# Kernel tuning notes

Hardware: AMD Instinct MI355X
Metric: run time of the kernel (lower is better)

The kernel has to match this reference:

```python
import jax, jax.numpy as jnp
import numpy as np
import math

DIM = 1024
HEADS = 16
DIM_HEAD = 64
INNER = HEADS * DIM_HEAD
NUM_BUCKETS = 32
MAX_DISTANCE = 128


def setup_inputs() -> dict:
    key = jax.random.key(0)
    ks = jax.random.split(key, 6)
    x = jax.random.normal(ks[0], (2, 2048, DIM), dtype=jnp.float32)
    Wq = jax.random.normal(ks[1], (DIM, INNER), dtype=jnp.float32) * (DIM ** -0.5)
    Wkv = jax.random.normal(ks[2], (DIM, 2 * DIM_HEAD), dtype=jnp.float32) * (DIM ** -0.5)
    Wout = jax.random.normal(ks[3], (INNER, DIM), dtype=jnp.float32) * (INNER ** -0.5)
    bout = jnp.zeros((DIM,), dtype=jnp.float32)
    rel_emb = jax.random.normal(ks[4], (NUM_BUCKETS, HEADS), dtype=jnp.float32) * 0.02
    return {"x": x, "Wq": Wq, "Wkv": Wkv, "Wout": Wout, "bout": bout, "rel_emb": rel_emb}


def _relative_position_bucket(rel_pos, num_buckets=NUM_BUCKETS, max_distance=MAX_DISTANCE):
    # rel_pos: [i, j] int32, k_pos - q_pos
    n = jnp.maximum(-rel_pos, 0)
    max_exact = num_buckets // 2
    is_small = n < max_exact
    n_safe = jnp.maximum(n, 1)  # avoid log(0); masked by is_small anyway
    val_if_large = max_exact + (
        jnp.log(n_safe.astype(jnp.float32) / max_exact)
        / math.log(max_distance / max_exact)
        * (num_buckets - max_exact)
    ).astype(jnp.int32)
    val_if_large = jnp.minimum(val_if_large, num_buckets - 1)
    return jnp.where(is_small, n, val_if_large)


def reference(x, Wq, Wkv, Wout, bout, rel_emb):
    b, n, _ = x.shape
    scale = DIM_HEAD ** -0.5
    bias_scale = DIM_HEAD ** 0.5

    q = (x @ Wq).reshape(b, n, HEADS, DIM_HEAD).transpose(0, 2, 1, 3) * scale  # [b,h,n,d]
    kv = x @ Wkv  # [b,n,2d]
    k, v = kv[..., :DIM_HEAD], kv[..., DIM_HEAD:]  # shared single-head K/V [b,n,d]

    sim = jnp.einsum('bhid,bjd->bhij', q, k)

    # T5 relative position bias
    pos = jnp.arange(n, dtype=jnp.int32)
    rel_pos = pos[None, :] - pos[:, None]  # [i,j] = k_pos - q_pos
    rp_bucket = _relative_position_bucket(rel_pos)
    bias = rel_emb[rp_bucket]  # [i,j,h]
    sim = sim + jnp.transpose(bias, (2, 0, 1))[None] * bias_scale

    # causal mask: mask strictly-upper triangle
    causal_mask = jnp.triu(jnp.ones((n, n), dtype=bool), k=1)
    neg = jnp.finfo(sim.dtype).max
    sim = jnp.where(causal_mask[None, None], -neg, sim)

    attn = jax.nn.softmax(sim, axis=-1)
    out = jnp.einsum('bhij,bjd->bhid', attn, v)
    out = out.transpose(0, 2, 1, 3).reshape(b, n, INNER)
    return out @ Wout + bout
```

## Files before the change

### kernel.cpp

```cpp
#include <hip/hip_runtime.h>
#include <cstdint>
#include <cmath>

typedef _Float16 half8 __attribute__((ext_vector_type(8)));
typedef unsigned short ushort8 __attribute__((ext_vector_type(8)));
typedef float floatx4 __attribute__((ext_vector_type(4)));

#define VT_STRIDE 2080

__device__ __forceinline__ unsigned short f2h(float f) {
    union { _Float16 h; unsigned short u; } cv;
    cv.h = (_Float16)f;
    return cv.u;
}

__device__ __forceinline__ void gld_lds16(const unsigned short* g, unsigned short* l) {
    __builtin_amdgcn_global_load_lds(
        (const __attribute__((address_space(1))) unsigned int*)g,
        (__attribute__((address_space(3))) unsigned int*)l, 16, 0, 0);
}

__global__ void prep_kernel(const float* __restrict__ x,
                            const float* __restrict__ Wq, const float* __restrict__ Wkv,
                            const float* __restrict__ Wout,
                            unsigned short* __restrict__ xh,
                            unsigned short* __restrict__ Wqkvt, unsigned short* __restrict__ Wot) {
    int bxi = blockIdx.x;
    if (bxi >= 68) {
        int fb = (bxi - 68) * 32 + blockIdx.y;
        int tt = threadIdx.y * 32 + threadIdx.x;
        int idx = fb * 256 + tt;
        const float4* p = (const float4*)x;
        float4 a = p[idx * 2], b = p[idx * 2 + 1];
        ushort8 o;
        o[0] = f2h(a.x); o[1] = f2h(a.y); o[2] = f2h(a.z); o[3] = f2h(a.w);
        o[4] = f2h(b.x); o[5] = f2h(b.y); o[6] = f2h(b.z); o[7] = f2h(b.w);
        *(ushort8*)(xh + (size_t)idx * 8) = o;
        return;
    }
    __shared__ float tile[32][33];
    const float* in; unsigned short* out; int C; int cb;
    if (bxi < 32)      { in = Wq;   out = Wqkvt;                 C = 1024; cb = bxi; }
    else if (bxi < 36) { in = Wkv;  out = Wqkvt + 1024 * 1024;   C = 128;  cb = bxi - 32; }
    else               { in = Wout; out = Wot;                   C = 1024; cb = bxi - 36; }
    int bx = cb * 32, by = blockIdx.y * 32;
    int xx = threadIdx.x, y0 = threadIdx.y;
    #pragma unroll
    for (int k = 0; k < 4; k++) {
        int y = y0 + k * 8;
        tile[y][xx] = in[(size_t)(by + y) * C + bx + xx];
    }
    __syncthreads();
    #pragma unroll
    for (int k = 0; k < 4; k++) {
        int y = y0 + k * 8;
        out[(size_t)(bx + y) * 1024 + by + xx] = f2h(tile[xx][y]);
    }
}

template<int MODE>
__global__ __launch_bounds__(256) void gemm_mn(
    const unsigned short* __restrict__ A, const unsigned short* __restrict__ Bt,
    unsigned short* __restrict__ oq, unsigned short* __restrict__ ok,
    unsigned short* __restrict__ ov, float* __restrict__ of,
    const float* __restrict__ bias)
{
    __shared__ __align__(16) unsigned short As[2][64 * 64];
    __shared__ __align__(16) unsigned short Bs[2][64 * 64];
    const int K = 1024;
    int t = threadIdx.x;
    int w = t >> 6, lane = t & 63, g = lane >> 4, il = lane & 15;
    int wr = w >> 1, wc = w & 1;
    int m0 = blockIdx.x * 64, n0 = blockIdx.y * 64;

    int l8 = lane >> 3, b8 = lane & 7;
    int swz = (b8 ^ l8) * 8;
    const unsigned short* Ag = A  + (size_t)(m0 + w * 16 + l8) * K + swz;
    const unsigned short* Bg = Bt + (size_t)(n0 + w * 16 + l8) * K + swz;
    int e0 = (g ^ (il & 7)) * 8;

    floatx4 acc[2][2] = {};

    #pragma unroll
    for (int q = 0; q < 2; q++) {
        gld_lds16(Ag + (size_t)(q * 8) * K, &As[0][(w * 16 + q * 8) * 64]);
        gld_lds16(Bg + (size_t)(q * 8) * K, &Bs[0][(w * 16 + q * 8) * 64]);
    }

    int cb = 0;
    for (int k0 = 0; k0 < K; k0 += 64, cb ^= 1) {
        if (k0 + 64 < K) {
            #pragma unroll
            for (int q = 0; q < 2; q++) {
                gld_lds16(Ag + (size_t)(q * 8) * K + k0 + 64, &As[cb ^ 1][(w * 16 + q * 8) * 64]);
                gld_lds16(Bg + (size_t)(q * 8) * K + k0 + 64, &Bs[cb ^ 1][(w * 16 + q * 8) * 64]);
            }
            asm volatile("s_waitcnt vmcnt(4)" ::: "memory");
        } else {
            asm volatile("s_waitcnt vmcnt(0)" ::: "memory");
        }
        __builtin_amdgcn_s_barrier();
        __builtin_amdgcn_sched_barrier(0);

        const unsigned short* Ac = &As[cb][0];
        const unsigned short* Bc = &Bs[cb][0];
        #pragma unroll
        for (int ks = 0; ks < 2; ks++) {
            half8 a[2];
            #pragma unroll
            for (int mt = 0; mt < 2; mt++)
                a[mt] = *(const half8*)&Ac[(wr * 32 + mt * 16 + il) * 64 + (e0 ^ (ks * 32))];
            #pragma unroll
            for (int nt = 0; nt < 2; nt++) {
                half8 b = *(const half8*)&Bc[(wc * 32 + nt * 16 + il) * 64 + (e0 ^ (ks * 32))];
                #pragma unroll
                for (int mt = 0; mt < 2; mt++)
                    acc[mt][nt] = __builtin_amdgcn_mfma_f32_16x16x32_f16(a[mt], b, acc[mt][nt], 0, 0, 0);
            }
        }
        asm volatile("s_waitcnt lgkmcnt(0)" ::: "memory");
        __builtin_amdgcn_s_barrier();
    }

    #pragma unroll
    for (int mt = 0; mt < 2; mt++) {
        #pragma unroll
        for (int nt = 0; nt < 2; nt++) {
            #pragma unroll
            for (int r = 0; r < 4; r++) {
                int row = m0 + wr * 32 + mt * 16 + 4 * g + r;
                int col = n0 + wc * 32 + nt * 16 + il;
                float v = acc[mt][nt][r];
                if (MODE == 0) {
                    if (col < 1024) {
                        int b = row >> 11, i = row & 2047, h = col >> 6, d = col & 63;
                        oq[(size_t)((b * 16 + h) * 2048 + i) * 64 + d] = f2h(v * 0.18033688011112042f);
                    } else if (col < 1088) {
                        ok[(size_t)row * 64 + (col - 1024)] = f2h(v);
                    } else {
                        int b = row >> 11, j = row & 2047;
                        ov[(size_t)((b << 6) + (col - 1088)) * VT_STRIDE + j] = f2h(v);
                    }
                } else {
                    of[(size_t)row * 1024 + col] = v + bias[col];
                }
            }
        }
    }
}

__global__ __launch_bounds__(256) void attn_kernel(
    const unsigned short* __restrict__ qh, const unsigned short* __restrict__ kh,
    const unsigned short* __restrict__ vt, const float* __restrict__ rel_emb,
    unsigned short* __restrict__ ob)
{
    __shared__ float bias_tab[256];
    __shared__ __align__(16) unsigned short Ks[2][64 * 64];
    __shared__ __align__(16) unsigned short Vs[64 * 64];
    __shared__ __align__(16) unsigned short Pl[64 * 72];

    int bx = 31 - blockIdx.y;
    int bh = blockIdx.x;
    int b = bh >> 4, h = bh & 15;
    int t = threadIdx.x;
    int w = t >> 6, lane = t & 63, g = lane >> 4, il = lane & 15;

    {
        int dlt = t;
        int bucket;
        if (dlt < 16) bucket = dlt;
        else {
            float lg = logf((float)dlt * 0.0625f) / 2.0794415416798357f;
            int vv = 16 + (int)(lg * 16.0f);
            bucket = vv < 31 ? vv : 31;
        }
        bias_tab[dlt] = rel_emb[bucket * 16 + h] * 11.541560327111708f;
    }
    float cb31 = rel_emb[31 * 16 + h] * 11.541560327111708f;

    const unsigned short* kbase = kh + (size_t)b * (2048 * 64);
    const unsigned short* vbase = vt + (size_t)b * (64 * VT_STRIDE);
    int prow = (w * 16 + il) * 72;

    int l8 = lane >> 3, b8 = lane & 7;
    int swz = (b8 ^ l8) * 8;
    const unsigned short* kg_base = kbase + (size_t)(w * 16 + l8) * 64 + swz;
    const unsigned short* vg_base = vbase + (size_t)(w * 16 + l8) * VT_STRIDE + swz;
    int e0 = (g ^ (il & 7)) * 8;

    int iw = bx * 64 + w * 16;
    int i_glob = iw + il;
    const unsigned short* qrow = qh + (size_t)(bh * 2048 + i_glob) * 64;
    half8 qf0 = *(const half8*)(qrow + g * 8);
    half8 qf1 = *(const half8*)(qrow + 32 + g * 8);
    floatx4 O[4] = {};
    float m_run = -1e30f, l_run = 0.0f;

    gld_lds16(kg_base,                 &Ks[0][(w * 16) * 64]);
    gld_lds16(kg_base + 8 * 64,        &Ks[0][(w * 16 + 8) * 64]);
    gld_lds16(vg_base,                 &Vs[(w * 16) * 64]);
    gld_lds16(vg_base + 8 * VT_STRIDE, &Vs[(w * 16 + 8) * 64]);

    for (int c = 0; c <= bx; c++) {
        __syncthreads();
        if (c < bx) {
            const unsigned short* kg = kg_base + (size_t)(c + 1) * 4096;
            unsigned short* kd = &Ks[(c + 1) & 1][0];
            gld_lds16(kg,          &kd[(w * 16) * 64]);
            gld_lds16(kg + 8 * 64, &kd[(w * 16 + 8) * 64]);
        }
        const unsigned short* Kc = &Ks[c & 1][0];
        int j0 = c * 64;

        floatx4 S[4] = {};
        __builtin_amdgcn_s_setprio(1);
        #pragma unroll
        for (int jt = 0; jt < 4; jt++) {
            half8 k0 = *(const half8*)&Kc[jt * 1024 + il * 64 + e0];
            half8 k1 = *(const half8*)&Kc[jt * 1024 + il * 64 + (e0 ^ 32)];
            S[jt] = __builtin_amdgcn_mfma_f32_16x16x32_f16(k0, qf0, S[jt], 0, 0, 0);
            S[jt] = __builtin_amdgcn_mfma_f32_16x16x32_f16(k1, qf1, S[jt], 0, 0, 0);
        }
        __builtin_amdgcn_s_setprio(0);
        half8 vf[8];
        #pragma unroll
        for (int ks = 0; ks < 2; ks++)
            #pragma unroll
            for (int dt = 0; dt < 4; dt++)
                vf[ks * 4 + dt] = *(const half8*)&Vs[dt * 1024 + il * 64 + (e0 ^ (ks * 32))];

        asm volatile("s_waitcnt lgkmcnt(0)" ::: "memory");
        __builtin_amdgcn_s_barrier();
        if (c < bx) {
            const unsigned short* vg = vg_base + (c + 1) * 64;
            gld_lds16(vg,                 &Vs[(w * 16) * 64]);
            gld_lds16(vg + 8 * VT_STRIDE, &Vs[(w * 16 + 8) * 64]);
        }

        float s[16];
        if (c + 3 <= bx) {
            #pragma unroll
            for (int q2 = 0; q2 < 16; q2++) s[q2] = S[q2 >> 2][q2 & 3] + cb31;
        } else if (c < bx) {
            #pragma unroll
            for (int jt = 0; jt < 4; jt++)
                #pragma unroll
                for (int r = 0; r < 4; r++)
                    s[jt * 4 + r] = S[jt][r] + bias_tab[i_glob - (j0 + jt * 16 + 4 * g + r)];
        } else {
            #pragma unroll
            for (int jt = 0; jt < 4; jt++) {
                #pragma unroll
                for (int r = 0; r < 4; r++) {
                    int delta = i_glob - (j0 + jt * 16 + 4 * g + r);
                    int di = delta > 0 ? delta : 0;
                    s[jt * 4 + r] = (delta >= 0) ? (S[jt][r] + bias_tab[di]) : -1e30f;
                }
            }
        }
        float m8[8];
        #pragma unroll
        for (int q2 = 0; q2 < 8; q2++) m8[q2] = fmaxf(s[q2], s[q2 + 8]);
        #pragma unroll
        for (int q2 = 0; q2 < 4; q2++) m8[q2] = fmaxf(m8[q2], m8[q2 + 4]);
        float mx = fmaxf(fmaxf(m8[0], m8[1]), fmaxf(m8[2], m8[3]));
        mx = fmaxf(mx, __shfl_xor(mx, 16));
        mx = fmaxf(mx, __shfl_xor(mx, 32));
        float m_new = fmaxf(m_run, mx);
        float alpha = __builtin_amdgcn_exp2f(m_run - m_new);
        float p[16];
        #pragma unroll
        for (int q2 = 0; q2 < 16; q2++) p[q2] = __builtin_amdgcn_exp2f(s[q2] - m_new);
        float ps[8];
        #pragma unroll
        for (int q2 = 0; q2 < 8; q2++) ps[q2] = p[q2] + p[q2 + 8];
        #pragma unroll
        for (int q2 = 0; q2 < 4; q2++) ps[q2] += ps[q2 + 4];
        float psum = (ps[0] + ps[1]) + (ps[2] + ps[3]);
        psum += __shfl_xor(psum, 16);
        psum += __shfl_xor(psum, 32);
        l_run = l_run * alpha + psum;
        m_run = m_new;
        float arow[4];
        #pragma unroll
        for (int r = 0; r < 4; r++) arow[r] = __shfl(alpha, 4 * g + r);
        #pragma unroll
        for (int dt = 0; dt < 4; dt++)
            #pragma unroll
            for (int r = 0; r < 4; r++) O[dt][r] *= arow[r];

        #pragma unroll
        for (int jt = 0; jt < 4; jt++) {
            uint2 u;
            u.x = (unsigned int)f2h(p[jt * 4 + 0]) | ((unsigned int)f2h(p[jt * 4 + 1]) << 16);
            u.y = (unsigned int)f2h(p[jt * 4 + 2]) | ((unsigned int)f2h(p[jt * 4 + 3]) << 16);
            *(uint2*)&Pl[prow + jt * 16 + 4 * g] = u;
        }
        __builtin_amdgcn_s_setprio(1);
        #pragma unroll
        for (int ks = 0; ks < 2; ks++) {
            half8 pf = *(const half8*)&Pl[prow + ks * 32 + g * 8];
            #pragma unroll
            for (int dt = 0; dt < 4; dt++)
                O[dt] = __builtin_amdgcn_mfma_f32_16x16x32_f16(pf, vf[ks * 4 + dt], O[dt], 0, 0, 0);
        }
        __builtin_amdgcn_s_setprio(0);
    }
    float inv[4];
    #pragma unroll
    for (int r = 0; r < 4; r++) inv[r] = 1.0f / __shfl(l_run, 4 * g + r);
    #pragma unroll
    for (int dt = 0; dt < 4; dt++) {
        #pragma unroll
        for (int r = 0; r < 4; r++) {
            int i = iw + 4 * g + r;
            int d = dt * 16 + il;
            ob[(size_t)(b * 2048 + i) * 1024 + h * 64 + d] = f2h(O[dt][r] * inv[r]);
        }
    }
}

extern "C" void kernel_launch(void* const* d_in, const int* in_sizes, int n_in,
                              void* d_out, int out_size, void* d_ws, size_t ws_size,
                              hipStream_t stream) {
    const float* x    = (const float*)d_in[0];
    const float* Wq   = (const float*)d_in[1];
    const float* Wkv  = (const float*)d_in[2];
    const float* Wout = (const float*)d_in[3];
    const float* bout = (const float*)d_in[4];
    const float* rel  = (const float*)d_in[5];
    float* out = (float*)d_out;

    unsigned short* ws    = (unsigned short*)d_ws;
    unsigned short* xh    = ws;
    unsigned short* qh    = xh + 4194304;
    unsigned short* kh    = qh + 4194304;
    unsigned short* vt    = kh + 262144;
    unsigned short* Wqkvt = vt + 2 * 64 * VT_STRIDE;
    unsigned short* Wot   = Wqkvt + 1179648;
    unsigned short* ob    = xh;

    prep_kernel<<<dim3(132, 32), dim3(32, 8), 0, stream>>>(x, Wq, Wkv, Wout, xh, Wqkvt, Wot);
    gemm_mn<0><<<dim3(64, 18), 256, 0, stream>>>(xh, Wqkvt, qh, kh, vt, nullptr, nullptr);
    attn_kernel<<<dim3(32, 32), 256, 0, stream>>>(qh, kh, vt, rel, ob);
    gemm_mn<2><<<dim3(64, 16), 256, 0, stream>>>(ob, Wot, nullptr, nullptr, nullptr, out, bout);
}
```

Measured before the change: 168.2 us.

## Triple-buffer GEMM LDS tiles and drop setprio in attention loop

Moves the projection GEMM from double to triple buffering of its LDS tiles. It prefetches two k-steps ahead, with a matching vmcnt wait depth, so global-to-LDS loads have more time to land before they are needed. B fragments are now loaded together before the MFMA block, and the s_setprio hints around the attention MFMAs are removed. The trade-off is 50% more LDS per GEMM block, which may lower occupancy, and losing the priority hints may change how waves interleave in the attention kernel.

```diff
diff --git a/kernel.cpp b/kernel.cpp
--- a/kernel.cpp
+++ b/kernel.cpp
@@ -65,8 +65,8 @@
     unsigned short* __restrict__ ov, float* __restrict__ of,
     const float* __restrict__ bias)
 {
-    __shared__ __align__(16) unsigned short As[2][64 * 64];
-    __shared__ __align__(16) unsigned short Bs[2][64 * 64];
+    __shared__ __align__(16) unsigned short As[3][64 * 64];
+    __shared__ __align__(16) unsigned short Bs[3][64 * 64];
     const int K = 1024;
     int t = threadIdx.x;
     int w = t >> 6, lane = t & 63, g = lane >> 4, il = lane & 15;
@@ -83,18 +83,26 @@
 
     #pragma unroll
     for (int q = 0; q < 2; q++) {
-        gld_lds16(Ag + (size_t)(q * 8) * K, &As[0][(w * 16 + q * 8) * 64]);
-        gld_lds16(Bg + (size_t)(q * 8) * K, &Bs[0][(w * 16 + q * 8) * 64]);
-    }
-
-    int cb = 0;
-    for (int k0 = 0; k0 < K; k0 += 64, cb ^= 1) {
-        if (k0 + 64 < K) {
+        gld_lds16(Ag + (size_t)(q * 8) * K,      &As[0][(w * 16 + q * 8) * 64]);
+        gld_lds16(Bg + (size_t)(q * 8) * K,      &Bs[0][(w * 16 + q * 8) * 64]);
+    }
+    #pragma unroll
+    for (int q = 0; q < 2; q++) {
+        gld_lds16(Ag + (size_t)(q * 8) * K + 64, &As[1][(w * 16 + q * 8) * 64]);
+        gld_lds16(Bg + (size_t)(q * 8) * K + 64, &Bs[1][(w * 16 + q * 8) * 64]);
+    }
+
+    int cur = 0;
+    for (int k0 = 0; k0 < K; k0 += 64) {
+        int pf = cur ? cur - 1 : 2;
+        if (k0 + 128 < K) {
             #pragma unroll
             for (int q = 0; q < 2; q++) {
-                gld_lds16(Ag + (size_t)(q * 8) * K + k0 + 64, &As[cb ^ 1][(w * 16 + q * 8) * 64]);
-                gld_lds16(Bg + (size_t)(q * 8) * K + k0 + 64, &Bs[cb ^ 1][(w * 16 + q * 8) * 64]);
+                gld_lds16(Ag + (size_t)(q * 8) * K + k0 + 128, &As[pf][(w * 16 + q * 8) * 64]);
+                gld_lds16(Bg + (size_t)(q * 8) * K + k0 + 128, &Bs[pf][(w * 16 + q * 8) * 64]);
             }
+            asm volatile("s_waitcnt vmcnt(8)" ::: "memory");
+        } else if (k0 + 64 < K) {
             asm volatile("s_waitcnt vmcnt(4)" ::: "memory");
         } else {
             asm volatile("s_waitcnt vmcnt(0)" ::: "memory");
@@ -102,24 +110,26 @@
         __builtin_amdgcn_s_barrier();
         __builtin_amdgcn_sched_barrier(0);
 
-        const unsigned short* Ac = &As[cb][0];
-        const unsigned short* Bc = &Bs[cb][0];
+        const unsigned short* Ac = &As[cur][0];
+        const unsigned short* Bc = &Bs[cur][0];
         #pragma unroll
         for (int ks = 0; ks < 2; ks++) {
-            half8 a[2];
+            half8 a[2], bfr[2];
             #pragma unroll
             for (int mt = 0; mt < 2; mt++)
                 a[mt] = *(const half8*)&Ac[(wr * 32 + mt * 16 + il) * 64 + (e0 ^ (ks * 32))];
             #pragma unroll
-            for (int nt = 0; nt < 2; nt++) {
-                half8 b = *(const half8*)&Bc[(wc * 32 + nt * 16 + il) * 64 + (e0 ^ (ks * 32))];
+            for (int nt = 0; nt < 2; nt++)
+                bfr[nt] = *(const half8*)&Bc[(wc * 32 + nt * 16 + il) * 64 + (e0 ^ (ks * 32))];
+            #pragma unroll
+            for (int nt = 0; nt < 2; nt++)
                 #pragma unroll
                 for (int mt = 0; mt < 2; mt++)
-                    acc[mt][nt] = __builtin_amdgcn_mfma_f32_16x16x32_f16(a[mt], b, acc[mt][nt], 0, 0, 0);
-            }
+                    acc[mt][nt] = __builtin_amdgcn_mfma_f32_16x16x32_f16(a[mt], bfr[nt], acc[mt][nt], 0, 0, 0);
         }
         asm volatile("s_waitcnt lgkmcnt(0)" ::: "memory");
         __builtin_amdgcn_s_barrier();
+        cur = cur == 2 ? 0 : cur + 1;
     }
 
     #pragma unroll
@@ -213,7 +223,6 @@
         int j0 = c * 64;
 
         floatx4 S[4] = {};
-        __builtin_amdgcn_s_setprio(1);
         #pragma unroll
         for (int jt = 0; jt < 4; jt++) {
             half8 k0 = *(const half8*)&Kc[jt * 1024 + il * 64 + e0];
@@ -221,7 +230,6 @@
             S[jt] = __builtin_amdgcn_mfma_f32_16x16x32_f16(k0, qf0, S[jt], 0, 0, 0);
             S[jt] = __builtin_amdgcn_mfma_f32_16x16x32_f16(k1, qf1, S[jt], 0, 0, 0);
         }
-        __builtin_amdgcn_s_setprio(0);
         half8 vf[8];
         #pragma unroll
         for (int ks = 0; ks < 2; ks++)
@@ -296,7 +304,6 @@
             u.y = (unsigned int)f2h(p[jt * 4 + 2]) | ((unsigned int)f2h(p[jt * 4 + 3]) << 16);
             *(uint2*)&Pl[prow + jt * 16 + 4 * g] = u;
         }
-        __builtin_amdgcn_s_setprio(1);
         #pragma unroll
         for (int ks = 0; ks < 2; ks++) {
             half8 pf = *(const half8*)&Pl[prow + ks * 32 + g * 8];
@@ -304,7 +311,6 @@
             for (int dt = 0; dt < 4; dt++)
                 O[dt] = __builtin_amdgcn_mfma_f32_16x16x32_f16(pf, vf[ks * 4 + dt], O[dt], 0, 0, 0);
         }
-        __builtin_amdgcn_s_setprio(0);
     }
     float inv[4];
     #pragma unroll
```

After: 171.4 us. About the same (+1.9%).
